# Kernel tuning notes

Hardware: AMD Instinct MI355X
Metric: run time of the kernel (lower is better)

Reference implementation:

```python
import jax, jax.numpy as jnp
import numpy as np

B, N, F, E, D = 2, 50000, 128, 800000, 4


def setup_inputs() -> dict:
    key = jax.random.key(0)
    ks = jax.random.split(key, 6)
    X = jax.random.normal(ks[0], (B, N, F), dtype=jnp.float32)
    u_val = jax.random.normal(ks[1], (E, D), dtype=jnp.float32)
    u_rows = jax.random.randint(ks[2], (E,), 0, N, dtype=jnp.int32)
    u_cols = jax.random.randint(ks[3], (E,), 0, N, dtype=jnp.int32)
    mu = jax.random.uniform(ks[4], (1, D), minval=-0.05, maxval=0.05, dtype=jnp.float32)
    # sigma kept away from 0 so sigma^2 in the denominator is numerically sane
    sigma = jax.random.uniform(ks[5], (1, D), minval=0.5, maxval=1.5, dtype=jnp.float32)
    return {"X": X, "u_val": u_val, "u_rows": u_rows, "u_cols": u_cols,
            "mu": mu, "sigma": sigma, "u_shape": N}


def reference(X, u_val, u_rows, u_cols, mu, sigma, u_shape):
    n = u_shape  # python int, static
    # per-edge Gaussian kernel log-weight: -0.5 * sum_d (u-mu)^2 / (sigma^2+eps)
    w = -0.5 * jnp.sum(jnp.square(u_val - mu) / (jnp.square(sigma) + 1e-14), axis=1)  # [E]
    # sparse (segment) softmax over rows == tf.sparse.softmax on reordered SparseTensor
    m = jax.ops.segment_max(w, u_rows, num_segments=n)          # [N]
    e = jnp.exp(w - m[u_rows])                                  # [E]
    s = jax.ops.segment_sum(e, u_rows, num_segments=n)          # [N]
    sm = e / s[u_rows]                                          # [E]
    # sparse-dense matmul: D[b,i,f] = sum_{edges e: row=i} sm_e * X[b, col_e, f]
    Xt = jnp.transpose(X, (1, 0, 2))                            # [N,B,F]
    msg = sm[:, None, None] * Xt[u_cols]                        # [E,B,F]
    Dn = jax.ops.segment_sum(msg, u_rows, num_segments=n)       # [N,B,F]
    return jnp.transpose(Dn, (1, 0, 2))                         # [B,N,F]
```

## Files before the change

### kernel.cpp

```cpp
#include <hip/hip_runtime.h>

constexpr int Bc = 2;
constexpr int Fc = 128;
constexpr int F4 = Fc / 4;
constexpr int EPT = 8;
constexpr int BIN_EDGES = 256 * EPT;
constexpr int CAP_MAX = 6144;

typedef float vfloat4 __attribute__((ext_vector_type(4)));

__device__ __forceinline__ unsigned short f2bf(float f) {
    unsigned u = __float_as_uint(f);
    unsigned r = (u + 0x7FFFu + ((u >> 16) & 1u)) >> 16;
    return (unsigned short)r;
}
__device__ __forceinline__ float bf2f(unsigned short h) {
    return __uint_as_float(((unsigned)h) << 16);
}
__device__ __forceinline__ void nt_store4(float4 v, float4* p) {
    vfloat4 q = {v.x, v.y, v.z, v.w};
    __builtin_nontemporal_store(q, (vfloat4*)p);
}
__device__ __forceinline__ float4 nt_load4(const float4* p) {
    vfloat4 q = __builtin_nontemporal_load((const vfloat4*)p);
    float4 r; r.x = q.x; r.y = q.y; r.z = q.z; r.w = q.w;
    return r;
}

__device__ __forceinline__ int block_incl_scan256(int v, int* wsum, int t) {
    int lane = t & 63, w = t >> 6;
    #pragma unroll
    for (int d = 1; d < 64; d <<= 1) {
        int u = __shfl_up(v, d);
        if (lane >= d) v += u;
    }
    if (lane == 63) wsum[w] = v;
    __syncthreads();
    int add = 0;
    #pragma unroll
    for (int i = 0; i < 3; ++i) if (i < w) add += wsum[i];
    return v + add;
}

__global__ __launch_bounds__(256) void prep_kernel(const float4* __restrict__ uval,
                                                   const float* __restrict__ mu,
                                                   const float* __restrict__ sigma,
                                                   const int* __restrict__ rows,
                                                   const int* __restrict__ cols,
                                                   int2* __restrict__ bucket_buf,
                                                   int* __restrict__ bucket_cursor,
                                                   const float4* __restrict__ X4,
                                                   ushort4* __restrict__ Xb,
                                                   int E, int N, int cap, int nbuk,
                                                   int nbin) {
    __shared__ int hist[256];
    __shared__ int excl[256];
    __shared__ int fill[256];
    __shared__ int chunkb[256];
    __shared__ int wsum[4];
    __shared__ int2 staged[BIN_EDGES];

    int t = threadIdx.x;

    if (blockIdx.x >= nbin) {
        long idx = (long)(blockIdx.x - nbin) * 256 + t;
        long tot = (long)Bc * N * F4;
        if (idx < tot) {
            int b  = (int)(idx / ((long)N * F4));
            int nt_ = (int)(idx - (long)b * N * F4);
            int n  = nt_ >> 5;
            int f4 = nt_ & 31;
            float4 v = nt_load4(&X4[(size_t)b * N * F4 + nt_]);
            ushort4 o;
            o.x = f2bf(v.x); o.y = f2bf(v.y); o.z = f2bf(v.z); o.w = f2bf(v.w);
            Xb[(size_t)n * (Bc * F4) + b * F4 + f4] = o;
        }
        return;
    }

    hist[t] = 0;
    float m0 = mu[0], m1 = mu[1], m2 = mu[2], m3 = mu[3];
    float i0 = 1.0f / (sigma[0] * sigma[0] + 1e-14f);
    float i1 = 1.0f / (sigma[1] * sigma[1] + 1e-14f);
    float i2 = 1.0f / (sigma[2] * sigma[2] + 1e-14f);
    float i3 = 1.0f / (sigma[3] * sigma[3] + 1e-14f);
    __syncthreads();

    int e0 = blockIdx.x * BIN_EDGES;
    int meta_r[EPT];
    float ev_r[EPT];
    int buk_r[EPT];
    #pragma unroll
    for (int it = 0; it < EPT; ++it) {
        int e = e0 + it * 256 + t;
        if (e < E) {
            int r = rows[e];
            int c = cols[e];
            float4 u = nt_load4((const float4*)&uval[e]);
            float d0 = u.x - m0, d1 = u.y - m1, d2 = u.z - m2, d3 = u.w - m3;
            float w = -0.5f * (d0 * d0 * i0 + d1 * d1 * i1 + d2 * d2 * i2 + d3 * d3 * i3);
            ev_r[it]   = expf(w);
            meta_r[it] = (r << 16) | c;
            buk_r[it]  = r >> 8;
            atomicAdd(&hist[buk_r[it]], 1);
        } else {
            buk_r[it] = -1;
        }
    }
    __syncthreads();

    int v = hist[t];
    int incl = block_incl_scan256(v, wsum, t);
    int ex = incl - v;
    excl[t] = ex;
    fill[t] = ex;
    if (t < nbuk && v > 0) chunkb[t] = atomicAdd(&bucket_cursor[t], v);
    __syncthreads();

    #pragma unroll
    for (int it = 0; it < EPT; ++it) {
        if (buk_r[it] >= 0) {
            int rk = atomicAdd(&fill[buk_r[it]], 1);
            staged[rk] = make_int2(meta_r[it], __float_as_int(ev_r[it]));
        }
    }
    __syncthreads();

    int nst = min(BIN_EDGES, E - e0);
    for (int k = t; k < nst; k += 256) {
        int2 x = staged[k];
        int buk = ((unsigned)x.x) >> 24;
        int rel = chunkb[buk] + (k - excl[buk]);
        if (rel < cap)
            bucket_buf[(size_t)buk * cap + rel] = x;
    }
}

__global__ __launch_bounds__(1024) void csr_kernel(const int2* __restrict__ bucket_buf,
                                                   const int* __restrict__ bucket_cursor,
                                                   int2* __restrict__ pairs,
                                                   int* __restrict__ rowstart,
                                                   int cap, int N, int nbuk) {
    __shared__ int sh[256];
    __shared__ int cur[256];
    __shared__ int wsum[4];
    __shared__ int2 staged[CAP_MAX];
    int b = blockIdx.x;
    int t = threadIdx.x;
    int lane = t & 63, w = t >> 6;

    int vA = 0, sA = 0;
    if (t < 256) {
        vA = (t < nbuk) ? min(bucket_cursor[t], cap) : 0;
        sA = vA;
        #pragma unroll
        for (int d = 1; d < 64; d <<= 1) {
            int u = __shfl_up(sA, d);
            if (lane >= d) sA += u;
        }
        if (lane == 63) wsum[w] = sA;
    }
    __syncthreads();
    if (t < 256) {
        int add = 0;
        #pragma unroll
        for (int i = 0; i < 3; ++i) if (i < w) add += wsum[i];
        sh[t] = sA + add;
    }
    __syncthreads();
    int cbase = (b == 0) ? 0 : sh[b - 1];
    int size  = min(bucket_cursor[b], cap);
    if (b == 0 && t == 0) rowstart[N] = sh[nbuk - 1];
    __syncthreads();

    if (t < 256) cur[t] = 0;
    __syncthreads();
    int base = b * cap;
    for (int k = t; k < size; k += 1024) {
        unsigned m = (unsigned)bucket_buf[base + k].x;
        atomicAdd(&cur[(m >> 16) & 0xFF], 1);
    }
    __syncthreads();

    int vC = 0, sC = 0;
    if (t < 256) {
        vC = cur[t];
        sC = vC;
        #pragma unroll
        for (int d = 1; d < 64; d <<= 1) {
            int u = __shfl_up(sC, d);
            if (lane >= d) sC += u;
        }
        if (lane == 63) wsum[w] = sC;
    }
    __syncthreads();
    if (t < 256) {
        int add = 0;
        #pragma unroll
        for (int i = 0; i < 3; ++i) if (i < w) add += wsum[i];
        int ex = sC + add - vC;
        cur[t] = ex;
        int row = b * 256 + t;
        if (row < N) rowstart[row] = cbase + ex;
    }
    __syncthreads();

    for (int k = t; k < size; k += 1024) {
        int2 x = bucket_buf[base + k];
        unsigned m = (unsigned)x.x;
        int rk = atomicAdd(&cur[(m >> 16) & 0xFF], 1);
        staged[rk] = make_int2((int)(m & 0xFFFFu), x.y);
    }
    __syncthreads();
    for (int k = t; k < size; k += 1024) pairs[cbase + k] = staged[k];
}

__global__ __launch_bounds__(64) void spmm_bf16(const ushort4* __restrict__ Xb,
                                                const int2* __restrict__ pairs,
                                                const int* __restrict__ rowstart,
                                                float4* __restrict__ out4, int N) {
    int lane = threadIdx.x;
    int i = blockIdx.x;
    int start = rowstart[i];
    int end   = rowstart[i + 1];
    int len   = end - start;
    float4 acc = {0.f, 0.f, 0.f, 0.f};
    float sum = 0.f;
    for (int c = 0; c < len; c += 64) {
        int m = min(64, len - c);
        int2 myp = make_int2(0, 0);
        if (lane < m) myp = pairs[start + c + lane];
        for (int g = 0; g < m; g += 8) {
            const ushort4* rp[8];
            float evv[8];
            #pragma unroll
            for (int e = 0; e < 8; ++e) {
                int col = __builtin_amdgcn_readlane(myp.x, g + e);
                evv[e]  = __uint_as_float((unsigned)__builtin_amdgcn_readlane(myp.y, g + e));
                rp[e]   = Xb + (size_t)col * 64;
            }
            ushort4 xs[8];
            #pragma unroll
            for (int e = 0; e < 8; ++e)
                xs[e] = rp[e][lane];
            #pragma unroll
            for (int e = 0; e < 8; ++e) {
                float ev = evv[e];
                sum += ev;
                acc.x = fmaf(ev, bf2f(xs[e].x), acc.x);
                acc.y = fmaf(ev, bf2f(xs[e].y), acc.y);
                acc.z = fmaf(ev, bf2f(xs[e].z), acc.z);
                acc.w = fmaf(ev, bf2f(xs[e].w), acc.w);
            }
        }
    }
    if (len > 0) {
        float inv = 1.0f / sum;
        acc.x *= inv; acc.y *= inv; acc.z *= inv; acc.w *= inv;
    }
    int b  = lane >> 5;
    int f4 = lane & 31;
    nt_store4(acc, &out4[(size_t)b * N * F4 + (size_t)i * F4 + f4]);
}

__global__ __launch_bounds__(64) void spmm_f32(const float4* __restrict__ X4,
                                               const int2* __restrict__ pairs,
                                               const int* __restrict__ rowstart,
                                               float4* __restrict__ out4, int N) {
    int lane = threadIdx.x;
    int i = blockIdx.x;
    int start = rowstart[i];
    int end   = rowstart[i + 1];
    int b  = lane >> 5;
    int f4 = lane & 31;
    float4 acc = {0.f, 0.f, 0.f, 0.f};
    float sum = 0.f;
    if (start < end) {
        int xbase = b * N * F4 + f4;
        for (int j = start; j < end; ++j) {
            int2 p = pairs[j];
            float ev = __int_as_float(p.y);
            sum += ev;
            float4 x = X4[xbase + (size_t)p.x * F4];
            acc.x = fmaf(ev, x.x, acc.x);
            acc.y = fmaf(ev, x.y, acc.y);
            acc.z = fmaf(ev, x.z, acc.z);
            acc.w = fmaf(ev, x.w, acc.w);
        }
        float inv = 1.0f / sum;
        acc.x *= inv; acc.y *= inv; acc.z *= inv; acc.w *= inv;
    }
    nt_store4(acc, &out4[(size_t)b * N * F4 + (size_t)i * F4 + f4]);
}

extern "C" void kernel_launch(void* const* d_in, const int* in_sizes, int n_in,
                              void* d_out, int out_size, void* d_ws, size_t ws_size,
                              hipStream_t stream) {
    const float* X      = (const float*)d_in[0];
    const float* u_val  = (const float*)d_in[1];
    const int*   u_rows = (const int*)d_in[2];
    const int*   u_cols = (const int*)d_in[3];
    const float* mu     = (const float*)d_in[4];
    const float* sigma  = (const float*)d_in[5];

    const int E = in_sizes[2];
    const int N = in_sizes[0] / (Bc * Fc);
    const int nbuk = (N + 255) >> 8;

    size_t off = 0;
    auto carve = [&](size_t bytes) -> char* {
        char* p = (char*)d_ws + off;
        off = (off + bytes + 255) & ~(size_t)255;
        return p;
    };
    int*  bucket_cursor = (int*)carve(256 * 4);
    int*  rowstart      = (int*)carve((size_t)(N + 1) * 4);
    int2* pairs         = (int2*)carve((size_t)E * 8);

    size_t xb_bytes = (size_t)N * Bc * Fc * 2;
    size_t avail    = (ws_size > off) ? (ws_size - off) : 0;
    int cap = CAP_MAX;
    size_t buck_bytes = (size_t)nbuk * cap * 8;
    if (buck_bytes + 512 > avail) {
        cap = (int)((avail - 512) / ((size_t)nbuk * 8));
        buck_bytes = (size_t)nbuk * cap * 8;
    }
    int2* bucket_buf = (int2*)carve(buck_bytes);
    bool use_bf16 = (off + xb_bytes) <= ws_size;
    ushort4* Xb = use_bf16 ? (ushort4*)carve(xb_bytes) : nullptr;

    hipMemsetAsync(bucket_cursor, 0, 256 * 4, stream);

    const int nbin  = (E + BIN_EDGES - 1) / BIN_EDGES;
    const int nconv = use_bf16 ? (int)(((long)Bc * N * F4 + 255) / 256) : 0;
    prep_kernel<<<nbin + nconv, 256, 0, stream>>>(
        (const float4*)u_val, mu, sigma, u_rows, u_cols,
        bucket_buf, bucket_cursor, (const float4*)X, Xb,
        E, N, cap, nbuk, nbin);
    csr_kernel<<<nbuk, 1024, 0, stream>>>(bucket_buf, bucket_cursor,
                                          pairs, rowstart, cap, N, nbuk);
    if (use_bf16) {
        spmm_bf16<<<N, 64, 0, stream>>>(Xb, pairs, rowstart, (float4*)d_out, N);
    } else {
        spmm_f32<<<N, 64, 0, stream>>>((const float4*)X, pairs, rowstart,
                                       (float4*)d_out, N);
    }
}
```

Baseline: 97.76 us.

## Fuse CSR bucketing and bf16 SpMM into one kernel using LDS-staged pairs

Merges the CSR build and the bf16 SpMM into a single kernel per 256-row bucket. Each 1024-thread block sorts its bucket's edges into shared memory, then each of its 16 wavefronts processes 16 rows directly from LDS. This removes the global pairs/rowstart round trip and one kernel launch. In exchange, parallelism drops from N 64-thread blocks to about 196 large blocks with heavy LDS use, which risks poor occupancy and load imbalance across rows.

```diff
diff --git a/kernel.cpp b/kernel.cpp
--- a/kernel.cpp
+++ b/kernel.cpp
@@ -136,6 +136,105 @@
     }
 }
 
+__global__ __launch_bounds__(1024) void csr_spmm_bf16(const int2* __restrict__ bucket_buf,
+                                                      const int* __restrict__ bucket_cursor,
+                                                      const ushort4* __restrict__ Xb,
+                                                      float4* __restrict__ out4,
+                                                      int cap, int N) {
+    __shared__ int hist[256];
+    __shared__ int excl[257];
+    __shared__ int wsum[4];
+    __shared__ int2 staged[CAP_MAX];
+    int b = blockIdx.x;
+    int t = threadIdx.x;
+    int lane = t & 63, w = t >> 6;
+
+    int size = min(bucket_cursor[b], cap);
+    int base = b * cap;
+
+    if (t < 256) hist[t] = 0;
+    __syncthreads();
+    for (int k = t; k < size; k += 1024) {
+        unsigned m = (unsigned)bucket_buf[base + k].x;
+        atomicAdd(&hist[(m >> 16) & 0xFF], 1);
+    }
+    __syncthreads();
+    int vC = 0, sC = 0;
+    if (t < 256) {
+        vC = hist[t];
+        sC = vC;
+        #pragma unroll
+        for (int d = 1; d < 64; d <<= 1) {
+            int u = __shfl_up(sC, d);
+            if (lane >= d) sC += u;
+        }
+        if (lane == 63) wsum[w] = sC;
+    }
+    __syncthreads();
+    if (t < 256) {
+        int add = 0;
+        #pragma unroll
+        for (int i = 0; i < 3; ++i) if (i < w) add += wsum[i];
+        excl[t] = sC + add - vC;
+    }
+    if (t == 0) excl[256] = size;
+    __syncthreads();
+    if (t < 256) hist[t] = excl[t];
+    __syncthreads();
+    for (int k = t; k < size; k += 1024) {
+        int2 x = bucket_buf[base + k];
+        unsigned m = (unsigned)x.x;
+        int rk = atomicAdd(&hist[(m >> 16) & 0xFF], 1);
+        staged[rk] = make_int2((int)(m & 0xFFFFu), x.y);
+    }
+    __syncthreads();
+
+    for (int q = 0; q < 16; ++q) {
+        int lr = w * 16 + q;
+        int i  = b * 256 + lr;
+        if (i >= N) break;
+        int start = excl[lr];
+        int len   = excl[lr + 1] - start;
+        float4 acc = {0.f, 0.f, 0.f, 0.f};
+        float sum = 0.f;
+        for (int c = 0; c < len; c += 64) {
+            int m = min(64, len - c);
+            int2 myp = make_int2(0, 0);
+            if (lane < m) myp = staged[start + c + lane];
+            for (int g = 0; g < m; g += 8) {
+                const ushort4* rp[8];
+                float evv[8];
+                #pragma unroll
+                for (int e = 0; e < 8; ++e) {
+                    int col = __builtin_amdgcn_readlane(myp.x, g + e);
+                    evv[e]  = __uint_as_float((unsigned)__builtin_amdgcn_readlane(myp.y, g + e));
+                    rp[e]   = Xb + (size_t)col * 64;
+                }
+                ushort4 xs[8];
+                #pragma unroll
+                for (int e = 0; e < 8; ++e)
+                    xs[e] = rp[e][lane];
+                #pragma unroll
+                for (int e = 0; e < 8; ++e) {
+                    float ev = evv[e];
+                    sum += ev;
+                    acc.x = fmaf(ev, bf2f(xs[e].x), acc.x);
+                    acc.y = fmaf(ev, bf2f(xs[e].y), acc.y);
+                    acc.z = fmaf(ev, bf2f(xs[e].z), acc.z);
+                    acc.w = fmaf(ev, bf2f(xs[e].w), acc.w);
+                }
+            }
+        }
+        if (len > 0) {
+            float inv = 1.0f / sum;
+            acc.x *= inv; acc.y *= inv; acc.z *= inv; acc.w *= inv;
+        }
+        int bb = lane >> 5;
+        int f4 = lane & 31;
+        nt_store4(acc, &out4[(size_t)bb * N * F4 + (size_t)i * F4 + f4]);
+    }
+}
+
 __global__ __launch_bounds__(1024) void csr_kernel(const int2* __restrict__ bucket_buf,
                                                    const int* __restrict__ bucket_cursor,
                                                    int2* __restrict__ pairs,
@@ -213,54 +312,6 @@
     }
     __syncthreads();
     for (int k = t; k < size; k += 1024) pairs[cbase + k] = staged[k];
-}
-
-__global__ __launch_bounds__(64) void spmm_bf16(const ushort4* __restrict__ Xb,
-                                                const int2* __restrict__ pairs,
-                                                const int* __restrict__ rowstart,
-                                                float4* __restrict__ out4, int N) {
-    int lane = threadIdx.x;
-    int i = blockIdx.x;
-    int start = rowstart[i];
-    int end   = rowstart[i + 1];
-    int len   = end - start;
-    float4 acc = {0.f, 0.f, 0.f, 0.f};
-    float sum = 0.f;
-    for (int c = 0; c < len; c += 64) {
-        int m = min(64, len - c);
-        int2 myp = make_int2(0, 0);
-        if (lane < m) myp = pairs[start + c + lane];
-        for (int g = 0; g < m; g += 8) {
-            const ushort4* rp[8];
-            float evv[8];
-            #pragma unroll
-            for (int e = 0; e < 8; ++e) {
-                int col = __builtin_amdgcn_readlane(myp.x, g + e);
-                evv[e]  = __uint_as_float((unsigned)__builtin_amdgcn_readlane(myp.y, g + e));
-                rp[e]   = Xb + (size_t)col * 64;
-            }
-            ushort4 xs[8];
-            #pragma unroll
-            for (int e = 0; e < 8; ++e)
-                xs[e] = rp[e][lane];
-            #pragma unroll
-            for (int e = 0; e < 8; ++e) {
-                float ev = evv[e];
-                sum += ev;
-                acc.x = fmaf(ev, bf2f(xs[e].x), acc.x);
-                acc.y = fmaf(ev, bf2f(xs[e].y), acc.y);
-                acc.z = fmaf(ev, bf2f(xs[e].z), acc.z);
-                acc.w = fmaf(ev, bf2f(xs[e].w), acc.w);
-            }
-        }
-    }
-    if (len > 0) {
-        float inv = 1.0f / sum;
-        acc.x *= inv; acc.y *= inv; acc.z *= inv; acc.w *= inv;
-    }
-    int b  = lane >> 5;
-    int f4 = lane & 31;
-    nt_store4(acc, &out4[(size_t)b * N * F4 + (size_t)i * F4 + f4]);
 }
 
 __global__ __launch_bounds__(64) void spmm_f32(const float4* __restrict__ X4,
@@ -337,11 +388,13 @@
         (const float4*)u_val, mu, sigma, u_rows, u_cols,
         bucket_buf, bucket_cursor, (const float4*)X, Xb,
         E, N, cap, nbuk, nbin);
-    csr_kernel<<<nbuk, 1024, 0, stream>>>(bucket_buf, bucket_cursor,
-                                          pairs, rowstart, cap, N, nbuk);
+
     if (use_bf16) {
-        spmm_bf16<<<N, 64, 0, stream>>>(Xb, pairs, rowstart, (float4*)d_out, N);
+        csr_spmm_bf16<<<nbuk, 1024, 0, stream>>>(
+            bucket_buf, bucket_cursor, Xb, (float4*)d_out, cap, N);
     } else {
+        csr_kernel<<<nbuk, 1024, 0, stream>>>(bucket_buf, bucket_cursor,
+                                              pairs, rowstart, cap, N, nbuk);
         spmm_f32<<<N, 64, 0, stream>>>((const float4*)X, pairs, rowstart,
                                        (float4*)d_out, N);
     }
```

New measurement: 97.75 us. Within noise of the previous version (-0.0%).
